# Kernel optimization log

Measured on AMD Instinct MI355X. Metric: run time of the kernel, lower is better.

## Reference

```python
import jax, jax.numpy as jnp
import numpy as np

N_NODES = 100000
N_EDGES = 1600000
IN_DIM, HID_DIM, OUT_DIM = 128, 32, 32
NEG_SLOPE = 0.2  # DGL GATConv default


def setup_inputs() -> dict:
    key = jax.random.key(0)
    ks = jax.random.split(key, 12)
    features = jax.random.normal(ks[0], (N_NODES, IN_DIM), dtype=jnp.float32)
    src = jax.random.randint(ks[1], (N_EDGES,), 0, N_NODES, dtype=jnp.int32)
    dst = jax.random.randint(ks[2], (N_EDGES,), 0, N_NODES, dtype=jnp.int32)
    s1 = 1.0 / np.sqrt(IN_DIM)
    s2 = 1.0 / np.sqrt(HID_DIM)
    W1 = jax.random.normal(ks[3], (IN_DIM, HID_DIM), dtype=jnp.float32) * s1
    al1 = jax.random.normal(ks[4], (HID_DIM,), dtype=jnp.float32) * s2
    ar1 = jax.random.normal(ks[5], (HID_DIM,), dtype=jnp.float32) * s2
    b1 = jnp.zeros((HID_DIM,), dtype=jnp.float32)
    W2 = jax.random.normal(ks[6], (HID_DIM, OUT_DIM), dtype=jnp.float32) * s2
    al2 = jax.random.normal(ks[7], (OUT_DIM,), dtype=jnp.float32) * s2
    ar2 = jax.random.normal(ks[8], (OUT_DIM,), dtype=jnp.float32) * s2
    b2 = jnp.zeros((OUT_DIM,), dtype=jnp.float32)
    return {"features": features, "src": src, "dst": dst,
            "W1": W1, "al1": al1, "ar1": ar1, "b1": b1,
            "W2": W2, "al2": al2, "ar2": ar2, "b2": b2}


def gat_conv(x, W, a_l, a_r, b, src, dst, n_nodes):
    # x: [N, Din] -> h: [N, D]
    h = x @ W
    el = h @ a_l  # [N] per-node left attention logit
    er = h @ a_r  # [N]
    # per-edge score with LeakyReLU (DGL default negative_slope=0.2)
    e = jax.nn.leaky_relu(el[src] + er[dst], negative_slope=NEG_SLOPE)  # [E]
    # segment softmax over edges grouped by destination node
    emax = jax.ops.segment_max(e, dst, num_segments=n_nodes)  # [N]
    ex = jnp.exp(e - emax[dst])  # [E]
    denom = jax.ops.segment_sum(ex, dst, num_segments=n_nodes)  # [N]
    alpha = ex / denom[dst]  # [E], every edge's dst has degree >= 1
    # scatter-weighted aggregation of source features
    out = jax.ops.segment_sum(h[src] * alpha[:, None], dst, num_segments=n_nodes)
    return out + b


def reference(features, src, dst, W1, al1, ar1, b1, W2, al2, ar2, b2):
    n = features.shape[0]
    h = gat_conv(features, W1, al1, ar1, b1, src, dst, n)
    h = jax.nn.elu(h)
    out = gat_conv(h, W2, al2, ar2, b2, src, dst, n)
    return out  # [N, OUT_DIM]
```

## Files before the change

### kernel.cpp

```cpp
#include <hip/hip_runtime.h>
#include <hip/hip_bf16.h>

#define N_NODES 100000
#define N_EDGES 1600000
#define IN_DIM 128
#define HID 32
#define BW 128
#define NBUCK ((N_NODES + BW - 1) / BW)
#define CAP 4096


using bf16x8 = __attribute__((ext_vector_type(8))) short;
using f32x4  = __attribute__((ext_vector_type(4))) float;

__device__ __forceinline__ short f2bf(float f) {
    return __builtin_bit_cast(short, __float2bfloat16(f));
}
__device__ __forceinline__ float bf2f(short s) {
    return __bfloat162float(__builtin_bit_cast(__hip_bfloat16, s));
}

__global__ __launch_bounds__(256) void gemm1_kernel(
    const float* __restrict__ x, const float* __restrict__ W,
    const float* __restrict__ al, const float* __restrict__ ar,
    __hip_bfloat16* __restrict__ h, float* __restrict__ el, float* __restrict__ er,
    int* __restrict__ gcur)
{
    __shared__ float Xs[64][132];
    const int tid = threadIdx.x;
    const int row0 = blockIdx.x * 64;

    const int gid = blockIdx.x * 256 + tid;
    if (gid < NBUCK) gcur[gid] = gid * CAP;

    const int lane = tid & 63, wid = tid >> 6;
    const int l15 = lane & 15, g = lane >> 4;

    bf16x8 bh[4][2], bl[4][2];
    #pragma unroll
    for (int q = 0; q < 4; ++q)
        #pragma unroll
        for (int ct = 0; ct < 2; ++ct)
            #pragma unroll
            for (int j = 0; j < 8; ++j) {
                const float wv = W[(32 * q + 8 * g + j) * HID + ct * 16 + l15];
                const short hi = f2bf(wv);
                bh[q][ct][j] = hi;
                bl[q][ct][j] = f2bf(wv - bf2f(hi));
            }

    #pragma unroll
    for (int i = 0; i < 8; ++i) {
        const int f = tid + 256 * i;
        const int r = f >> 5, c4 = f & 31;
        const int gr = row0 + r;
        float4 v = make_float4(0.f, 0.f, 0.f, 0.f);
        if (gr < N_NODES) v = ((const float4*)x)[(size_t)gr * 32 + c4];
        *(float4*)&Xs[r][c4 * 4] = v;
    }
    __syncthreads();

    const int tile = blockIdx.x * 4 + wid;
    if (tile * 16 >= N_NODES) return;
    const int rl = wid * 16 + l15;

    f32x4 acc0 = {0.f, 0.f, 0.f, 0.f}, acc1 = {0.f, 0.f, 0.f, 0.f};
    #pragma unroll
    for (int q = 0; q < 4; ++q) {
        const float4 xa = *(const float4*)&Xs[rl][32 * q + 8 * g];
        const float4 xb = *(const float4*)&Xs[rl][32 * q + 8 * g + 4];
        const float xs[8] = {xa.x, xa.y, xa.z, xa.w, xb.x, xb.y, xb.z, xb.w};
        bf16x8 ah, alo;
        #pragma unroll
        for (int j = 0; j < 8; ++j) {
            const short hi = f2bf(xs[j]);
            ah[j] = hi;
            alo[j] = f2bf(xs[j] - bf2f(hi));
        }
        acc0 = __builtin_amdgcn_mfma_f32_16x16x32_bf16(ah,  bh[q][0], acc0, 0, 0, 0);
        acc0 = __builtin_amdgcn_mfma_f32_16x16x32_bf16(alo, bh[q][0], acc0, 0, 0, 0);
        acc0 = __builtin_amdgcn_mfma_f32_16x16x32_bf16(ah,  bl[q][0], acc0, 0, 0, 0);
        acc1 = __builtin_amdgcn_mfma_f32_16x16x32_bf16(ah,  bh[q][1], acc1, 0, 0, 0);
        acc1 = __builtin_amdgcn_mfma_f32_16x16x32_bf16(alo, bh[q][1], acc1, 0, 0, 0);
        acc1 = __builtin_amdgcn_mfma_f32_16x16x32_bf16(ah,  bl[q][1], acc1, 0, 0, 0);
    }

    const int grow0 = tile * 16 + 4 * g;
    const float a0 = al[l15], a1 = al[16 + l15];
    const float r0 = ar[l15], r1 = ar[16 + l15];
    float pel[4], per_[4];
    #pragma unroll
    for (int i = 0; i < 4; ++i) {
        const int grow = grow0 + i;
        h[(size_t)grow * HID + l15]      = __float2bfloat16(acc0[i]);
        h[(size_t)grow * HID + 16 + l15] = __float2bfloat16(acc1[i]);
        pel[i]  = acc0[i] * a0 + acc1[i] * a1;
        per_[i] = acc0[i] * r0 + acc1[i] * r1;
    }
    #pragma unroll
    for (int m = 1; m < 16; m <<= 1)
        #pragma unroll
        for (int i = 0; i < 4; ++i) {
            pel[i]  += __shfl_xor(pel[i],  m, 16);
            per_[i] += __shfl_xor(per_[i], m, 16);
        }
    if (l15 == 0)
        #pragma unroll
        for (int i = 0; i < 4; ++i) { el[grow0 + i] = pel[i]; er[grow0 + i] = per_[i]; }
}

__global__ __launch_bounds__(256) void bin_kernel(const int* __restrict__ src,
                                                  const int* __restrict__ dst,
                                                  int* __restrict__ gcur,
                                                  int* __restrict__ pairs)
{
    __shared__ int hist[NBUCK];
    __shared__ int cur[NBUCK];
    const int tid = threadIdx.x;
    for (int i = tid; i < NBUCK; i += 256) hist[i] = 0;
    __syncthreads();

    const int t = blockIdx.x * 256 + tid;
    const bool act = t < N_EDGES / 16;
    int4 sv[4], dv[4];
    if (act) {
        const int4* s4 = (const int4*)src + (size_t)t * 4;
        const int4* d4 = (const int4*)dst + (size_t)t * 4;
        #pragma unroll
        for (int q = 0; q < 4; ++q) { sv[q] = s4[q]; dv[q] = d4[q]; }
        #pragma unroll
        for (int q = 0; q < 4; ++q) {
            atomicAdd(&hist[dv[q].x >> 7], 1); atomicAdd(&hist[dv[q].y >> 7], 1);
            atomicAdd(&hist[dv[q].z >> 7], 1); atomicAdd(&hist[dv[q].w >> 7], 1);
        }
    }
    __syncthreads();
    for (int i = tid; i < NBUCK; i += 256) {
        const int hv = hist[i];
        cur[i] = hv ? atomicAdd(&gcur[i], hv) : 0;
    }
    __syncthreads();
    if (act) {
        #pragma unroll
        for (int q = 0; q < 4; ++q) {
            const int ss[4] = {sv[q].x, sv[q].y, sv[q].z, sv[q].w};
            const int dd[4] = {dv[q].x, dv[q].y, dv[q].z, dv[q].w};
            #pragma unroll
            for (int r = 0; r < 4; ++r) {
                const int slot = atomicAdd(&cur[dd[r] >> 7], 1);
                pairs[slot] = (ss[r] << 7) | (dd[r] & (BW - 1));
            }
        }
    }
}

__global__ __launch_bounds__(256) void lsort_kernel(
    const int* __restrict__ gcur, int* __restrict__ pairs,
    int* __restrict__ deg, int* __restrict__ rowptr)
{
    __shared__ int lp[CAP];
    __shared__ int lc[CAP];
    __shared__ int lhist[BW];
    __shared__ int lcur[BW];
    __shared__ int w0tot;
    const int tid = threadIdx.x;
    const int b = blockIdx.x;
    const int rbase = b * CAP;
    int ecnt = gcur[b] - rbase;
    if (ecnt > CAP) ecnt = CAP;
    if (tid < BW) lhist[tid] = 0;
    __syncthreads();
    for (int i = tid; i < ecnt; i += 256) {
        const int p = pairs[rbase + i];
        lp[i] = p;
        atomicAdd(&lhist[p & (BW - 1)], 1);
    }
    __syncthreads();
    const int lane = tid & 63;
    int v = 0;
    if (tid < BW) v = lhist[tid];
    int pre = v;
    #pragma unroll
    for (int off = 1; off < 64; off <<= 1) {
        const int n = __shfl_up(pre, off, 64);
        if (lane >= off) pre += n;
    }
    if (tid == 63) w0tot = pre;
    __syncthreads();
    if (tid < BW) {
        const int ex = pre - v + (tid >= 64 ? w0tot : 0);
        lcur[tid] = ex;
        const int node = b * BW + tid;
        if (node < N_NODES) { deg[node] = v; rowptr[node] = rbase + ex; }
    }
    __syncthreads();
    for (int i = tid; i < ecnt; i += 256) {
        const int p = lp[i];
        const int slot = atomicAdd(&lcur[p & (BW - 1)], 1);
        lc[slot] = p;
    }
    __syncthreads();
    for (int i = tid; i < ecnt; i += 256) pairs[rbase + i] = lc[i];
}

template <int MODE>
__global__ __launch_bounds__(256) void gather_kernel(
    const int* __restrict__ rowptr, const int* __restrict__ deg,
    const int* __restrict__ csr,
    const float* __restrict__ el, const float* __restrict__ er,
    const __hip_bfloat16* __restrict__ h, const float* __restrict__ bias,
    const float* __restrict__ W2, const float* __restrict__ al2,
    const float* __restrict__ ar2,
    __hip_bfloat16* __restrict__ h2, float* __restrict__ el2,
    float* __restrict__ er2, float* __restrict__ out)
{
    const int tid = threadIdx.x;
    float* W2s = nullptr;
    if constexpr (MODE == 0) {
        __shared__ float W2s_[HID * HID];
        W2s = W2s_;
        ((float4*)W2s)[tid] = ((const float4*)W2)[tid];
        __syncthreads();
    }
    const int node = blockIdx.x * 8 + (tid >> 5);
    const int col = tid & 31;
    const int cnt = deg[node];
    const int start = rowptr[node];
    const float erd = er[node];
    float acc = 0.f, denl = 0.f;
    for (int base = 0; base < cnt; base += 32) {
        const int rem = cnt - base;
        int p = 0; float wv = 0.f;
        if (col < rem) {
            p = csr[start + base + col];
            float sc = el[p >> 7] + erd;
            sc = sc > 0.f ? sc : 0.2f * sc;
            wv = __expf(sc);
        }
        denl += wv;
        const int m = rem < 32 ? rem : 32;
        int k = 0;
        for (; k + 3 < m; k += 4) {
            const int   p0 = __shfl(p, k, 32),     p1 = __shfl(p, k + 1, 32);
            const int   p2 = __shfl(p, k + 2, 32), p3 = __shfl(p, k + 3, 32);
            const float w0 = __shfl(wv, k, 32),     w1 = __shfl(wv, k + 1, 32);
            const float w2 = __shfl(wv, k + 2, 32), w3 = __shfl(wv, k + 3, 32);
            const float h0 = __bfloat162float(h[(size_t)(p0 >> 7) * HID + col]);
            const float h1 = __bfloat162float(h[(size_t)(p1 >> 7) * HID + col]);
            const float h2v = __bfloat162float(h[(size_t)(p2 >> 7) * HID + col]);
            const float h3 = __bfloat162float(h[(size_t)(p3 >> 7) * HID + col]);
            acc += w0 * h0 + w1 * h1 + w2 * h2v + w3 * h3;
        }
        for (; k < m; ++k) {
            const int pk = __shfl(p, k, 32);
            const float wk = __shfl(wv, k, 32);
            acc += wk * __bfloat162float(h[(size_t)(pk >> 7) * HID + col]);
        }
    }
    float den = denl;
    #pragma unroll
    for (int mm = 16; mm > 0; mm >>= 1) den += __shfl_xor(den, mm, 32);

    float v = den > 0.f ? acc / den : 0.f;
    v += bias[col];
    if constexpr (MODE == 0) {
        v = v > 0.f ? v : expm1f(v);
        float hacc = 0.f;
        #pragma unroll
        for (int k = 0; k < HID; ++k)
            hacc += __shfl(v, k, 32) * W2s[k * HID + col];
        h2[(size_t)node * HID + col] = __float2bfloat16(hacc);
        float pel = hacc * al2[col], per = hacc * ar2[col];
        #pragma unroll
        for (int mm = 16; mm > 0; mm >>= 1) {
            pel += __shfl_xor(pel, mm, 32);
            per += __shfl_xor(per, mm, 32);
        }
        if (col == 0) { el2[node] = pel; er2[node] = per; }
    } else {
        out[(size_t)node * HID + col] = v;
    }
}

extern "C" void kernel_launch(void* const* d_in, const int* in_sizes, int n_in,
                              void* d_out, int out_size, void* d_ws, size_t ws_size,
                              hipStream_t stream) {
    const float* features = (const float*)d_in[0];
    const int*   src      = (const int*)d_in[1];
    const int*   dst      = (const int*)d_in[2];
    const float* W1       = (const float*)d_in[3];
    const float* al1      = (const float*)d_in[4];
    const float* ar1      = (const float*)d_in[5];
    const float* b1       = (const float*)d_in[6];
    const float* W2       = (const float*)d_in[7];
    const float* al2      = (const float*)d_in[8];
    const float* ar2      = (const float*)d_in[9];
    const float* b2       = (const float*)d_in[10];
    float* out = (float*)d_out;

    int*  gcur   = (int*)d_ws;
    int*  deg    = gcur + 784;
    int*  rowptr = deg + N_NODES;
    int*  pairs  = rowptr + N_NODES;
    __hip_bfloat16* h1 = (__hip_bfloat16*)(pairs + NBUCK * CAP);
    float* el1 = (float*)(h1 + (size_t)N_NODES * HID);
    float* er1 = el1 + N_NODES;
    __hip_bfloat16* h2 = (__hip_bfloat16*)(er1 + N_NODES);
    float* el2 = (float*)(h2 + (size_t)N_NODES * HID);
    float* er2 = el2 + N_NODES;

    const int NB_E16 = (N_EDGES / 16 + 255) / 256;
    const int NB_G1  = (N_NODES + 63) / 64;

    gemm1_kernel<<<NB_G1, 256, 0, stream>>>(features, W1, al1, ar1,
                                            h1, el1, er1, gcur);
    bin_kernel<<<NB_E16, 256, 0, stream>>>(src, dst, gcur, pairs);
    lsort_kernel<<<NBUCK, 256, 0, stream>>>(gcur, pairs, deg, rowptr);
    gather_kernel<0><<<N_NODES / 8, 256, 0, stream>>>(rowptr, deg, pairs,
                                                      el1, er1, h1, b1,
                                                      W2, al2, ar2,
                                                      h2, el2, er2, nullptr);
    gather_kernel<1><<<N_NODES / 8, 256, 0, stream>>>(rowptr, deg, pairs,
                                                      el2, er2, h2, b2,
                                                      nullptr, nullptr, nullptr,
                                                      nullptr, nullptr, nullptr, out);
}
```

Measured before the change: 237.9 us.

## Precompute per-edge attention weights in sort pass and separate kernel

Edge attention weights exp(leakyrelu(el[src]+er[dst])) are now computed once per edge into a workspace buffer. For layer 1 this happens inside the local sort kernel, and for layer 2 a new wcalc kernel does it. The gather kernels then read contiguous weights instead of doing random el lookups, shuffles and exps, and the inner loop is restructured as a per-lane 8-way unrolled walk over the edge list. The bin kernel also moves to 512-thread blocks. The cost is an extra kernel launch and a full weight-buffer write and read per layer, while every lane in a 32-lane group now issues redundant broadcast loads of csr and w.

```diff
diff --git a/kernel.cpp b/kernel.cpp
--- a/kernel.cpp
+++ b/kernel.cpp
@@ -109,7 +109,7 @@
         for (int i = 0; i < 4; ++i) { el[grow0 + i] = pel[i]; er[grow0 + i] = per_[i]; }
 }
 
-__global__ __launch_bounds__(256) void bin_kernel(const int* __restrict__ src,
+__global__ __launch_bounds__(512) void bin_kernel(const int* __restrict__ src,
                                                   const int* __restrict__ dst,
                                                   int* __restrict__ gcur,
                                                   int* __restrict__ pairs)
@@ -117,10 +117,10 @@
     __shared__ int hist[NBUCK];
     __shared__ int cur[NBUCK];
     const int tid = threadIdx.x;
-    for (int i = tid; i < NBUCK; i += 256) hist[i] = 0;
-    __syncthreads();
-
-    const int t = blockIdx.x * 256 + tid;
+    for (int i = tid; i < NBUCK; i += 512) hist[i] = 0;
+    __syncthreads();
+
+    const int t = blockIdx.x * 512 + tid;
     const bool act = t < N_EDGES / 16;
     int4 sv[4], dv[4];
     if (act) {
@@ -135,7 +135,7 @@
         }
     }
     __syncthreads();
-    for (int i = tid; i < NBUCK; i += 256) {
+    for (int i = tid; i < NBUCK; i += 512) {
         const int hv = hist[i];
         cur[i] = hv ? atomicAdd(&gcur[i], hv) : 0;
     }
@@ -156,19 +156,25 @@
 
 __global__ __launch_bounds__(256) void lsort_kernel(
     const int* __restrict__ gcur, int* __restrict__ pairs,
-    int* __restrict__ deg, int* __restrict__ rowptr)
+    const float* __restrict__ el, const float* __restrict__ er,
+    int* __restrict__ deg, int* __restrict__ rowptr, float* __restrict__ w1)
 {
     __shared__ int lp[CAP];
     __shared__ int lc[CAP];
     __shared__ int lhist[BW];
     __shared__ int lcur[BW];
+    __shared__ float ers[BW];
     __shared__ int w0tot;
     const int tid = threadIdx.x;
     const int b = blockIdx.x;
     const int rbase = b * CAP;
+    const int node0 = b * BW;
     int ecnt = gcur[b] - rbase;
     if (ecnt > CAP) ecnt = CAP;
-    if (tid < BW) lhist[tid] = 0;
+    if (tid < BW) {
+        lhist[tid] = 0;
+        ers[tid] = (node0 + tid < N_NODES) ? er[node0 + tid] : 0.f;
+    }
     __syncthreads();
     for (int i = tid; i < ecnt; i += 256) {
         const int p = pairs[rbase + i];
@@ -190,7 +196,7 @@
     if (tid < BW) {
         const int ex = pre - v + (tid >= 64 ? w0tot : 0);
         lcur[tid] = ex;
-        const int node = b * BW + tid;
+        const int node = node0 + tid;
         if (node < N_NODES) { deg[node] = v; rowptr[node] = rbase + ex; }
     }
     __syncthreads();
@@ -200,14 +206,41 @@
         lc[slot] = p;
     }
     __syncthreads();
-    for (int i = tid; i < ecnt; i += 256) pairs[rbase + i] = lc[i];
+    for (int i = tid; i < ecnt; i += 256) {
+        const int p = lc[i];
+        pairs[rbase + i] = p;
+        float sc = el[p >> 7] + ers[p & (BW - 1)];
+        sc = sc > 0.f ? sc : 0.2f * sc;
+        w1[rbase + i] = __expf(sc);
+    }
+}
+
+__global__ __launch_bounds__(256) void wcalc_kernel(
+    const int* __restrict__ gcur, const int* __restrict__ csr,
+    const float* __restrict__ el, const float* __restrict__ er,
+    float* __restrict__ w)
+{
+    __shared__ float ers[BW];
+    const int tid = threadIdx.x;
+    const int b = blockIdx.x;
+    const int rbase = b * CAP;
+    const int node0 = b * BW;
+    if (tid < BW) ers[tid] = (node0 + tid < N_NODES) ? er[node0 + tid] : 0.f;
+    __syncthreads();
+    int ecnt = gcur[b] - rbase;
+    if (ecnt > CAP) ecnt = CAP;
+    for (int i = tid; i < ecnt; i += 256) {
+        const int p = csr[rbase + i];
+        float sc = el[p >> 7] + ers[p & (BW - 1)];
+        sc = sc > 0.f ? sc : 0.2f * sc;
+        w[rbase + i] = __expf(sc);
+    }
 }
 
 template <int MODE>
 __global__ __launch_bounds__(256) void gather_kernel(
     const int* __restrict__ rowptr, const int* __restrict__ deg,
-    const int* __restrict__ csr,
-    const float* __restrict__ el, const float* __restrict__ er,
+    const int* __restrict__ csr, const float* __restrict__ w,
     const __hip_bfloat16* __restrict__ h, const float* __restrict__ bias,
     const float* __restrict__ W2, const float* __restrict__ al2,
     const float* __restrict__ ar2,
@@ -226,40 +259,43 @@
     const int col = tid & 31;
     const int cnt = deg[node];
     const int start = rowptr[node];
-    const float erd = er[node];
-    float acc = 0.f, denl = 0.f;
-    for (int base = 0; base < cnt; base += 32) {
-        const int rem = cnt - base;
-        int p = 0; float wv = 0.f;
-        if (col < rem) {
-            p = csr[start + base + col];
-            float sc = el[p >> 7] + erd;
-            sc = sc > 0.f ? sc : 0.2f * sc;
-            wv = __expf(sc);
-        }
-        denl += wv;
-        const int m = rem < 32 ? rem : 32;
-        int k = 0;
-        for (; k + 3 < m; k += 4) {
-            const int   p0 = __shfl(p, k, 32),     p1 = __shfl(p, k + 1, 32);
-            const int   p2 = __shfl(p, k + 2, 32), p3 = __shfl(p, k + 3, 32);
-            const float w0 = __shfl(wv, k, 32),     w1 = __shfl(wv, k + 1, 32);
-            const float w2 = __shfl(wv, k + 2, 32), w3 = __shfl(wv, k + 3, 32);
-            const float h0 = __bfloat162float(h[(size_t)(p0 >> 7) * HID + col]);
-            const float h1 = __bfloat162float(h[(size_t)(p1 >> 7) * HID + col]);
-            const float h2v = __bfloat162float(h[(size_t)(p2 >> 7) * HID + col]);
-            const float h3 = __bfloat162float(h[(size_t)(p3 >> 7) * HID + col]);
-            acc += w0 * h0 + w1 * h1 + w2 * h2v + w3 * h3;
-        }
-        for (; k < m; ++k) {
-            const int pk = __shfl(p, k, 32);
-            const float wk = __shfl(wv, k, 32);
-            acc += wk * __bfloat162float(h[(size_t)(pk >> 7) * HID + col]);
-        }
-    }
-    float den = denl;
-    #pragma unroll
-    for (int mm = 16; mm > 0; mm >>= 1) den += __shfl_xor(den, mm, 32);
+    float acc = 0.f, den = 0.f;
+    int j = 0;
+    for (; j + 7 < cnt; j += 8) {
+        const int p0 = csr[start + j];
+        const int p1 = csr[start + j + 1];
+        const int p2 = csr[start + j + 2];
+        const int p3 = csr[start + j + 3];
+        const int p4 = csr[start + j + 4];
+        const int p5 = csr[start + j + 5];
+        const int p6 = csr[start + j + 6];
+        const int p7 = csr[start + j + 7];
+        const float w0 = w[start + j];
+        const float w1v = w[start + j + 1];
+        const float w2v = w[start + j + 2];
+        const float w3v = w[start + j + 3];
+        const float w4v = w[start + j + 4];
+        const float w5v = w[start + j + 5];
+        const float w6v = w[start + j + 6];
+        const float w7v = w[start + j + 7];
+        const float h0 = __bfloat162float(h[(size_t)(p0 >> 7) * HID + col]);
+        const float h1 = __bfloat162float(h[(size_t)(p1 >> 7) * HID + col]);
+        const float h2v = __bfloat162float(h[(size_t)(p2 >> 7) * HID + col]);
+        const float h3 = __bfloat162float(h[(size_t)(p3 >> 7) * HID + col]);
+        const float h4 = __bfloat162float(h[(size_t)(p4 >> 7) * HID + col]);
+        const float h5 = __bfloat162float(h[(size_t)(p5 >> 7) * HID + col]);
+        const float h6 = __bfloat162float(h[(size_t)(p6 >> 7) * HID + col]);
+        const float h7 = __bfloat162float(h[(size_t)(p7 >> 7) * HID + col]);
+        den += ((w0 + w1v) + (w2v + w3v)) + ((w4v + w5v) + (w6v + w7v));
+        acc += (w0 * h0 + w1v * h1 + w2v * h2v + w3v * h3)
+             + (w4v * h4 + w5v * h5 + w6v * h6 + w7v * h7);
+    }
+    for (; j < cnt; ++j) {
+        const int p = csr[start + j];
+        const float wv = w[start + j];
+        den += wv;
+        acc += wv * __bfloat162float(h[(size_t)(p >> 7) * HID + col]);
+    }
 
     float v = den > 0.f ? acc / den : 0.f;
     v += bias[col];
@@ -302,26 +338,28 @@
     int*  deg    = gcur + 784;
     int*  rowptr = deg + N_NODES;
     int*  pairs  = rowptr + N_NODES;
-    __hip_bfloat16* h1 = (__hip_bfloat16*)(pairs + NBUCK * CAP);
+    float* wbuf  = (float*)(pairs + NBUCK * CAP);
+    __hip_bfloat16* h1 = (__hip_bfloat16*)(wbuf + NBUCK * CAP);
     float* el1 = (float*)(h1 + (size_t)N_NODES * HID);
     float* er1 = el1 + N_NODES;
     __hip_bfloat16* h2 = (__hip_bfloat16*)(er1 + N_NODES);
     float* el2 = (float*)(h2 + (size_t)N_NODES * HID);
     float* er2 = el2 + N_NODES;
 
-    const int NB_E16 = (N_EDGES / 16 + 255) / 256;
+    const int NB_E16 = (N_EDGES / 16 + 511) / 512;
     const int NB_G1  = (N_NODES + 63) / 64;
 
     gemm1_kernel<<<NB_G1, 256, 0, stream>>>(features, W1, al1, ar1,
                                             h1, el1, er1, gcur);
-    bin_kernel<<<NB_E16, 256, 0, stream>>>(src, dst, gcur, pairs);
-    lsort_kernel<<<NBUCK, 256, 0, stream>>>(gcur, pairs, deg, rowptr);
-    gather_kernel<0><<<N_NODES / 8, 256, 0, stream>>>(rowptr, deg, pairs,
-                                                      el1, er1, h1, b1,
-                                                      W2, al2, ar2,
+    bin_kernel<<<NB_E16, 512, 0, stream>>>(src, dst, gcur, pairs);
+    lsort_kernel<<<NBUCK, 256, 0, stream>>>(gcur, pairs, el1, er1,
+                                            deg, rowptr, wbuf);
+    gather_kernel<0><<<N_NODES / 8, 256, 0, stream>>>(rowptr, deg, pairs, wbuf,
+                                                      h1, b1, W2, al2, ar2,
                                                       h2, el2, er2, nullptr);
-    gather_kernel<1><<<N_NODES / 8, 256, 0, stream>>>(rowptr, deg, pairs,
-                                                      el2, er2, h2, b2,
+    wcalc_kernel<<<NBUCK, 256, 0, stream>>>(gcur, pairs, el2, er2, wbuf);
+    gather_kernel<1><<<N_NODES / 8, 256, 0, stream>>>(rowptr, deg, pairs, wbuf,
+                                                      h2, b2,
                                                       nullptr, nullptr, nullptr,
                                                       nullptr, nullptr, nullptr, out);
 }
```

New measurement: 255.9 us. +7.6%, slower.
